# Kernel optimization log

Hardware: AMD Instinct MI355X
Metric: run time of the kernel (lower is better)

Reference implementation:

```python
import jax, jax.numpy as jnp
import numpy as np

ATOMF_LEN = 82
EDGE_DIM = 6
HIDDEN = 10
GNN_DEPTH = 2
N_NODES = 200000
N_EDGES = 6400000


def _lrelu(x):
    return jax.nn.leaky_relu(x, negative_slope=0.1)


def setup_inputs() -> dict:
    key = jax.random.key(0)
    ks = jax.random.split(key, 7)
    vertex = jax.random.normal(ks[0], (N_NODES, ATOMF_LEN), dtype=jnp.float32)
    edge_feat = jax.random.normal(ks[1], (N_EDGES, EDGE_DIM), dtype=jnp.float32)
    src = jax.random.randint(ks[2], (N_EDGES,), 0, N_NODES, dtype=jnp.int32)
    dst = jax.random.randint(ks[3], (N_EDGES,), 0, N_NODES, dtype=jnp.int32)
    # kaiming-uniform-ish init scale (fan_in based)
    weight_init = jax.random.uniform(ks[4], (ATOMF_LEN, HIDDEN), dtype=jnp.float32,
                                     minval=-1.0, maxval=1.0) * (np.sqrt(6.0 / ATOMF_LEN))
    gather_weight = jax.random.uniform(ks[5], (HIDDEN + EDGE_DIM, HIDDEN), dtype=jnp.float32,
                                       minval=-1.0, maxval=1.0) * (np.sqrt(6.0 / (HIDDEN + EDGE_DIM)))
    update_weight = jax.random.uniform(ks[6], (2 * HIDDEN, HIDDEN), dtype=jnp.float32,
                                       minval=-1.0, maxval=1.0) * (np.sqrt(6.0 / (2 * HIDDEN)))
    return {"vertex": vertex, "edge_feat": edge_feat, "src": src, "dst": dst,
            "weight_init": weight_init, "gather_weight": gather_weight,
            "update_weight": update_weight}


def reference(vertex, edge_feat, src, dst, weight_init, gather_weight, update_weight):
    # embedding_: leaky_relu(mm(x, W), 0.1)
    h = _lrelu(vertex @ weight_init)  # [N, HIDDEN]
    n_nodes = vertex.shape[0]
    for _ in range(GNN_DEPTH):
        # gather: per-edge message from source node hidden + edge features
        msg = _lrelu(jnp.concatenate([h[src], edge_feat], axis=1) @ gather_weight)  # [E, HIDDEN]
        # scatter-sum aggregation onto destination nodes
        agg = jax.ops.segment_sum(msg, dst, num_segments=n_nodes)  # [N, HIDDEN]
        # update: combine current hidden with aggregated messages
        h = _lrelu(jnp.concatenate([h, agg], axis=1) @ update_weight)  # [N, HIDDEN]
    return h
```

## Files before the change

kernel.cpp:

```cpp
#include <hip/hip_runtime.h>

#define ATOMF 82
#define EDGE_DIM 6
#define HIDDEN 10
#define ZPAD 16

#define BSHIFT 8
#define MAXBUCK 1024
#define NB1 1024
#define MAXE3 16384

__device__ __forceinline__ float lrelu(float x) { return x > 0.f ? x : 0.1f * x; }

__device__ __forceinline__ unsigned int f2bf(float f) {
    unsigned int u = __float_as_uint(f);
    return (u + 0x7fffu + ((u >> 16) & 1u)) >> 16;
}
__device__ __forceinline__ float bf2f(unsigned int b) {
    return __uint_as_float(b << 16);
}

__global__ void embed_kernel(const float* __restrict__ vertex,
                             const float* __restrict__ W,
                             const float* __restrict__ GW,
                             float* __restrict__ h, unsigned short* __restrict__ z,
                             int n_nodes) {
    __shared__ float w[ATOMF * HIDDEN];
    __shared__ float gwh[HIDDEN * HIDDEN];
    for (int i = threadIdx.x; i < ATOMF * HIDDEN; i += blockDim.x) w[i] = W[i];
    for (int i = threadIdx.x; i < HIDDEN * HIDDEN; i += blockDim.x) gwh[i] = GW[i];
    __syncthreads();
    int node = blockIdx.x * blockDim.x + threadIdx.x;
    if (node >= n_nodes) return;
    const float2* v = (const float2*)(vertex + (long)node * ATOMF);
    float acc[HIDDEN];
#pragma unroll
    for (int j = 0; j < HIDDEN; j++) acc[j] = 0.f;
#pragma unroll 2
    for (int k2 = 0; k2 < ATOMF / 2; k2++) {
        float2 t = v[k2];
#pragma unroll
        for (int j = 0; j < HIDDEN; j++) acc[j] += t.x * w[(2 * k2) * HIDDEN + j];
#pragma unroll
        for (int j = 0; j < HIDDEN; j++) acc[j] += t.y * w[(2 * k2 + 1) * HIDDEN + j];
    }
    float ho[HIDDEN];
    float* out = h + (long)node * HIDDEN;
#pragma unroll
    for (int j = 0; j < HIDDEN; j++) { ho[j] = lrelu(acc[j]); out[j] = ho[j]; }
    float zv[HIDDEN];
#pragma unroll
    for (int j = 0; j < HIDDEN; j++) zv[j] = 0.f;
#pragma unroll
    for (int k = 0; k < HIDDEN; k++) {
        float x = ho[k];
#pragma unroll
        for (int j = 0; j < HIDDEN; j++) zv[j] += x * gwh[k * HIDDEN + j];
    }
    unsigned int* zq = (unsigned int*)(z + (size_t)node * ZPAD);
    int4 pk;
    pk.x = (int)(f2bf(zv[0]) | (f2bf(zv[1]) << 16));
    pk.y = (int)(f2bf(zv[2]) | (f2bf(zv[3]) << 16));
    pk.z = (int)(f2bf(zv[4]) | (f2bf(zv[5]) << 16));
    pk.w = (int)(f2bf(zv[6]) | (f2bf(zv[7]) << 16));
    *(int4*)zq = pk;
    zq[4] = f2bf(zv[8]) | (f2bf(zv[9]) << 16);
}

__global__ __launch_bounds__(256) void hist_kernel(const int* __restrict__ dst,
                                                   int* __restrict__ hist,
                                                   long n_edges, int nbuck) {
    __shared__ int hl[MAXBUCK];
    for (int t = threadIdx.x; t < nbuck; t += 256) hl[t] = 0;
    __syncthreads();
    long per = (n_edges + gridDim.x - 1) / gridDim.x;
    long s = (long)blockIdx.x * per;
    long e = s + per; if (e > n_edges) e = n_edges;
    for (long i = s + threadIdx.x; i < e; i += 256)
        atomicAdd(&hl[dst[i] >> BSHIFT], 1);
    __syncthreads();
    for (int t = threadIdx.x; t < nbuck; t += 256)
        hist[(size_t)t * gridDim.x + blockIdx.x] = hl[t];
}

__global__ __launch_bounds__(1024) void scan_block_sums(const int* __restrict__ in,
                                                        int* __restrict__ partials, int n) {
    __shared__ int ws[16];
    int i = blockIdx.x * 1024 + threadIdx.x;
    int v = (i < n) ? in[i] : 0;
    int lane = threadIdx.x & 63, wid = threadIdx.x >> 6;
    int s = v;
#pragma unroll
    for (int off = 32; off > 0; off >>= 1) s += __shfl_down(s, off, 64);
    if (lane == 0) ws[wid] = s;
    __syncthreads();
    if (threadIdx.x == 0) {
        int t = 0;
#pragma unroll
        for (int k = 0; k < 16; k++) t += ws[k];
        partials[blockIdx.x] = t;
    }
}
__global__ __launch_bounds__(1024) void scan_partials(int* __restrict__ partials, int nb) {
    __shared__ int wsum[16];
    int lane = threadIdx.x & 63, wid = threadIdx.x >> 6;
    int v = (threadIdx.x < nb) ? partials[threadIdx.x] : 0;
    int incl = v;
#pragma unroll
    for (int off = 1; off < 64; off <<= 1) {
        int t = __shfl_up(incl, off, 64);
        if (lane >= off) incl += t;
    }
    if (lane == 63) wsum[wid] = incl;
    __syncthreads();
    if (wid == 0 && lane < 16) {
        int wv = wsum[lane];
        int wincl = wv;
#pragma unroll
        for (int off = 1; off < 16; off <<= 1) {
            int t = __shfl_up(wincl, off, 64);
            if (lane >= off) wincl += t;
        }
        wsum[lane] = wincl - wv;
    }
    __syncthreads();
    if (threadIdx.x < nb) partials[threadIdx.x] = wsum[wid] + (incl - v);
}
__global__ __launch_bounds__(1024) void scan_final(const int* __restrict__ in,
                                                   const int* __restrict__ partials,
                                                   int* __restrict__ out, int n) {
    __shared__ int wsum[16];
    int i = blockIdx.x * 1024 + threadIdx.x;
    int v = (i < n) ? in[i] : 0;
    int lane = threadIdx.x & 63, wid = threadIdx.x >> 6;
    int incl = v;
#pragma unroll
    for (int off = 1; off < 64; off <<= 1) {
        int t = __shfl_up(incl, off, 64);
        if (lane >= off) incl += t;
    }
    if (lane == 63) wsum[wid] = incl;
    __syncthreads();
    if (wid == 0 && lane < 16) {
        int wv = wsum[lane];
        int wincl = wv;
#pragma unroll
        for (int off = 1; off < 16; off <<= 1) {
            int t = __shfl_up(wincl, off, 64);
            if (lane >= off) wincl += t;
        }
        wsum[lane] = wincl - wv;
    }
    __syncthreads();
    if (i <= n) out[i] = partials[blockIdx.x] + wsum[wid] + (incl - v);
}

__global__ __launch_bounds__(256) void part_scatter_kernel(
    const int* __restrict__ src, const int* __restrict__ dst,
    const float* __restrict__ ef, const int* __restrict__ base,
    int4* __restrict__ rec_a, int* __restrict__ dst2,
    long n_edges, int nbuck) {
    __shared__ int cur[MAXBUCK];
    for (int t = threadIdx.x; t < nbuck; t += 256)
        cur[t] = base[(size_t)t * gridDim.x + blockIdx.x];
    __syncthreads();
    long per = (n_edges + gridDim.x - 1) / gridDim.x;
    long s = (long)blockIdx.x * per;
    long e = s + per; if (e > n_edges) e = n_edges;
    for (long i = s + threadIdx.x; i < e; i += 256) {
        int d = dst[i];
        int slot = atomicAdd(&cur[d >> BSHIFT], 1);
        const float2* er = (const float2*)(ef + i * (long)EDGE_DIM);
        float2 fa = er[0], fb = er[1], fc = er[2];
        int4 r;
        r.x = src[i];
        r.y = (int)(f2bf(fa.x) | (f2bf(fa.y) << 16));
        r.z = (int)(f2bf(fb.x) | (f2bf(fb.y) << 16));
        r.w = (int)(f2bf(fc.x) | (f2bf(fc.y) << 16));
        rec_a[slot] = r;
        dst2[slot] = d;
    }
}

__global__ __launch_bounds__(256) void bucket_csr_kernel(
    const int* __restrict__ base, const int* __restrict__ dst2,
    const int4* __restrict__ rec_a, int4* __restrict__ rec_b,
    int* __restrict__ offsets, int n_nodes) {
    __shared__ unsigned char lid[MAXE3];
    __shared__ int cnt[1 << BSHIFT];
    __shared__ int excl_s[1 << BSHIFT];
    __shared__ int cursor[1 << BSHIFT];
    int b = blockIdx.x;
    int S = base[(size_t)b * NB1];
    int E = base[(size_t)(b + 1) * NB1];
    int node0 = b << BSHIFT;
    int nn = n_nodes - node0; if (nn > (1 << BSHIFT)) nn = 1 << BSHIFT;
    cnt[threadIdx.x] = 0;
    __syncthreads();
    int ne = E - S;
    bool fit = (ne <= MAXE3);
    for (int i = threadIdx.x; i < ne; i += 256) {
        int l = dst2[S + i] - node0;
        if (fit) lid[i] = (unsigned char)l;
        atomicAdd(&cnt[l], 1);
    }
    __syncthreads();
    if (threadIdx.x == 0) {
        int run = 0;
#pragma unroll 4
        for (int l = 0; l < (1 << BSHIFT); l++) { excl_s[l] = run; run += cnt[l]; }
    }
    __syncthreads();
    if ((int)threadIdx.x < nn) offsets[node0 + threadIdx.x] = S + excl_s[threadIdx.x];
    cursor[threadIdx.x] = excl_s[threadIdx.x];
    if (b == (int)gridDim.x - 1 && threadIdx.x == 0) offsets[n_nodes] = E;
    __syncthreads();
    for (int i = threadIdx.x; i < ne; i += 256) {
        int l = fit ? (int)lid[i] : (dst2[S + i] - node0);
        int r = atomicAdd(&cursor[l], 1);
        rec_b[S + r] = rec_a[S + i];
    }
}

__global__ void count_pos_kernel(const int* __restrict__ dst, int* __restrict__ counts,
                                 unsigned short* __restrict__ pos, long n_edges) {
    long e0 = ((long)blockIdx.x * blockDim.x + threadIdx.x) * 4;
    if (e0 + 3 < n_edges) {
        int4 d = *(const int4*)(dst + e0);
        ushort4 p;
        p.x = (unsigned short)atomicAdd(&counts[d.x], 1);
        p.y = (unsigned short)atomicAdd(&counts[d.y], 1);
        p.z = (unsigned short)atomicAdd(&counts[d.z], 1);
        p.w = (unsigned short)atomicAdd(&counts[d.w], 1);
        *(ushort4*)(pos + e0) = p;
    } else {
        for (long e = e0; e < n_edges; e++)
            pos[e] = (unsigned short)atomicAdd(&counts[dst[e]], 1);
    }
}
__global__ void scatter_rec_kernel(const int* __restrict__ src, const int* __restrict__ dst,
                                   const float* __restrict__ ef,
                                   const unsigned short* __restrict__ pos,
                                   const int* __restrict__ offsets,
                                   int4* __restrict__ rec, long n_edges) {
    long e = (long)blockIdx.x * blockDim.x + threadIdx.x;
    if (e >= n_edges) return;
    int d = dst[e];
    int q = offsets[d] + (int)pos[e];
    const float2* er = (const float2*)(ef + e * (long)EDGE_DIM);
    float2 fa = er[0], fb = er[1], fc = er[2];
    int4 r;
    r.x = src[e];
    r.y = (int)(f2bf(fa.x) | (f2bf(fa.y) << 16));
    r.z = (int)(f2bf(fb.x) | (f2bf(fb.y) << 16));
    r.w = (int)(f2bf(fc.x) | (f2bf(fc.y) << 16));
    rec[q] = r;
}

__global__ __launch_bounds__(256) void gather_update_kernel(
    const float* __restrict__ h_in, const unsigned short* __restrict__ z_in,
    const int4* __restrict__ rec, const int* __restrict__ offsets,
    const float* __restrict__ GW, const float* __restrict__ UW,
    float* __restrict__ h_out, unsigned short* __restrict__ z_out,
    int n_nodes, int write_z) {
    __shared__ float gwh[HIDDEN * HIDDEN];
    __shared__ float gwe[EDGE_DIM * HIDDEN];
    __shared__ float uw[2 * HIDDEN * HIDDEN];
    for (int i = threadIdx.x; i < HIDDEN * HIDDEN; i += 256) gwh[i] = GW[i];
    for (int i = threadIdx.x; i < EDGE_DIM * HIDDEN; i += 256) gwe[i] = GW[HIDDEN * HIDDEN + i];
    for (int i = threadIdx.x; i < 2 * HIDDEN * HIDDEN; i += 256) uw[i] = UW[i];
    __syncthreads();
    int group = threadIdx.x >> 4;
    int sub = threadIdx.x & 15;
    int node = blockIdx.x * 16 + group;
    if (node >= n_nodes) return;
    int off0 = offsets[node], off1 = offsets[node + 1];
    float acc[HIDDEN];
#pragma unroll
    for (int j = 0; j < HIDDEN; j++) acc[j] = 0.f;
    int p = off0 + sub;
    int4 r;
    if (p < off1) r = rec[p];
    while (p < off1) {
        int pn = p + 16;
        int4 rn = r;
        if (pn < off1) rn = rec[pn];
        const int* zq = (const int*)(z_in + (size_t)r.x * ZPAD);
        int4 za = *(const int4*)zq;
        int zb = zq[4];
        float ef[EDGE_DIM];
        unsigned int u0 = (unsigned int)r.y, u1 = (unsigned int)r.z, u2 = (unsigned int)r.w;
        ef[0] = bf2f(u0 & 0xffffu); ef[1] = bf2f(u0 >> 16);
        ef[2] = bf2f(u1 & 0xffffu); ef[3] = bf2f(u1 >> 16);
        ef[4] = bf2f(u2 & 0xffffu); ef[5] = bf2f(u2 >> 16);
        float m[HIDDEN];
#pragma unroll
        for (int j = 0; j < HIDDEN; j++) m[j] = 0.f;
#pragma unroll
        for (int k = 0; k < EDGE_DIM; k++) {
            float x = ef[k];
#pragma unroll
            for (int j = 0; j < HIDDEN; j++) m[j] += x * gwe[k * HIDDEN + j];
        }
        unsigned int z0 = (unsigned int)za.x, z1 = (unsigned int)za.y;
        unsigned int z2 = (unsigned int)za.z, z3 = (unsigned int)za.w, z4 = (unsigned int)zb;
        acc[0] += lrelu(m[0] + bf2f(z0 & 0xffffu));
        acc[1] += lrelu(m[1] + bf2f(z0 >> 16));
        acc[2] += lrelu(m[2] + bf2f(z1 & 0xffffu));
        acc[3] += lrelu(m[3] + bf2f(z1 >> 16));
        acc[4] += lrelu(m[4] + bf2f(z2 & 0xffffu));
        acc[5] += lrelu(m[5] + bf2f(z2 >> 16));
        acc[6] += lrelu(m[6] + bf2f(z3 & 0xffffu));
        acc[7] += lrelu(m[7] + bf2f(z3 >> 16));
        acc[8] += lrelu(m[8] + bf2f(z4 & 0xffffu));
        acc[9] += lrelu(m[9] + bf2f(z4 >> 16));
        r = rn; p = pn;
    }
#pragma unroll
    for (int j = 0; j < HIDDEN; j++) {
#pragma unroll
        for (int d = 8; d > 0; d >>= 1) acc[j] += __shfl_down(acc[j], d, 16);
    }
    if (sub == 0) {
        float in[2 * HIDDEN];
        const float2* hp = (const float2*)(h_in + (long)node * HIDDEN);
#pragma unroll
        for (int k = 0; k < 5; k++) { float2 t = hp[k]; in[2 * k] = t.x; in[2 * k + 1] = t.y; }
#pragma unroll
        for (int j = 0; j < HIDDEN; j++) in[HIDDEN + j] = acc[j];
        float o[HIDDEN];
#pragma unroll
        for (int j = 0; j < HIDDEN; j++) o[j] = 0.f;
#pragma unroll
        for (int k = 0; k < 2 * HIDDEN; k++) {
            float x = in[k];
#pragma unroll
            for (int j = 0; j < HIDDEN; j++) o[j] += x * uw[k * HIDDEN + j];
        }
        float ho[HIDDEN];
        float* outp = h_out + (long)node * HIDDEN;
#pragma unroll
        for (int j = 0; j < HIDDEN; j++) { ho[j] = lrelu(o[j]); outp[j] = ho[j]; }
        if (write_z) {
            float zv[HIDDEN];
#pragma unroll
            for (int j = 0; j < HIDDEN; j++) zv[j] = 0.f;
#pragma unroll
            for (int k = 0; k < HIDDEN; k++) {
                float x = ho[k];
#pragma unroll
                for (int j = 0; j < HIDDEN; j++) zv[j] += x * gwh[k * HIDDEN + j];
            }
            unsigned int* zq = (unsigned int*)(z_out + (size_t)node * ZPAD);
            int4 pk;
            pk.x = (int)(f2bf(zv[0]) | (f2bf(zv[1]) << 16));
            pk.y = (int)(f2bf(zv[2]) | (f2bf(zv[3]) << 16));
            pk.z = (int)(f2bf(zv[4]) | (f2bf(zv[5]) << 16));
            pk.w = (int)(f2bf(zv[6]) | (f2bf(zv[7]) << 16));
            *(int4*)zq = pk;
            zq[4] = f2bf(zv[8]) | (f2bf(zv[9]) << 16);
        }
    }
}

extern "C" void kernel_launch(void* const* d_in, const int* in_sizes, int n_in,
                              void* d_out, int out_size, void* d_ws, size_t ws_size,
                              hipStream_t stream) {
    const float* vertex    = (const float*)d_in[0];
    const float* edge_feat = (const float*)d_in[1];
    const int*   src       = (const int*)d_in[2];
    const int*   dst       = (const int*)d_in[3];
    const float* w_init    = (const float*)d_in[4];
    const float* gw        = (const float*)d_in[5];
    const float* uw        = (const float*)d_in[6];

    const int  n_nodes = in_sizes[0] / ATOMF;
    const long n_edges = (long)in_sizes[2];
    float* out = (float*)d_out;

    const int TB = 256;
    const int node_blocks = (n_nodes + TB - 1) / TB;
    const int gu_blocks   = (n_nodes + 15) / 16;

    const int nbuck = (n_nodes + (1 << BSHIFT) - 1) >> BSHIFT;
    const long m = (long)nbuck * NB1;
    const int scanb_m = (int)((m + 1 + 1023) / 1024);

    size_t tbl_bytes = (size_t)n_nodes * (2 * HIDDEN * sizeof(float) + 2 * ZPAD * sizeof(unsigned short));
    size_t rec_bytes = (size_t)n_edges * sizeof(int4);

    auto al = [](size_t x) { return (x + 255) & ~(size_t)255; };
    size_t need_new = al(m * 4) + al((m + 1) * 4) + al(2048 * 4) +
                      al((size_t)(n_nodes + 1) * 4) + al(rec_bytes) +
                      al(rec_bytes > tbl_bytes ? rec_bytes : tbl_bytes) +
                      al((size_t)n_edges * 4);

    char* ws = (char*)d_ws;
    size_t o = 0;
    auto alloc = [&](size_t bytes) { char* p = ws + o; o = (o + bytes + 255) & ~(size_t)255; return p; };

    if (nbuck <= MAXBUCK && scanb_m <= 1024 && ws_size >= need_new) {
        int*  hist     = (int*)alloc(m * 4);
        int*  base     = (int*)alloc((m + 1) * 4);
        int*  partials = (int*)alloc(2048 * 4);
        int*  offsets  = (int*)alloc((size_t)(n_nodes + 1) * 4);
        int4* rec_b    = (int4*)alloc(rec_bytes);
        char* ovl      = alloc(rec_bytes > tbl_bytes ? rec_bytes : tbl_bytes);
        int4* rec_a    = (int4*)ovl;
        int*  dst2     = (int*)alloc((size_t)n_edges * 4);
        float*          h0 = (float*)ovl;
        float*          h1 = h0 + (size_t)n_nodes * HIDDEN;
        unsigned short* z0 = (unsigned short*)(h1 + (size_t)n_nodes * HIDDEN);
        unsigned short* z1 = z0 + (size_t)n_nodes * ZPAD;

        hipMemsetAsync(hist, 0, m * 4, stream);
        hist_kernel<<<NB1, 256, 0, stream>>>(dst, hist, n_edges, nbuck);
        scan_block_sums<<<scanb_m, 1024, 0, stream>>>(hist, partials, (int)m);
        scan_partials<<<1, 1024, 0, stream>>>(partials, scanb_m);
        scan_final<<<scanb_m, 1024, 0, stream>>>(hist, partials, base, (int)m);
        part_scatter_kernel<<<NB1, 256, 0, stream>>>(src, dst, edge_feat, base,
                                                     rec_a, dst2, n_edges, nbuck);
        bucket_csr_kernel<<<nbuck, 256, 0, stream>>>(base, dst2, rec_a, rec_b,
                                                     offsets, n_nodes);

        embed_kernel<<<node_blocks, TB, 0, stream>>>(vertex, w_init, gw, h0, z0, n_nodes);
        gather_update_kernel<<<gu_blocks, TB, 0, stream>>>(h0, z0, rec_b, offsets, gw, uw,
                                                           h1, z1, n_nodes, 1);
        gather_update_kernel<<<gu_blocks, TB, 0, stream>>>(h1, z1, rec_b, offsets, gw, uw,
                                                           out, z0, n_nodes, 0);
    } else {
        int*  counts   = (int*)alloc((size_t)(n_nodes + 1) * 4);
        int*  offsets  = (int*)alloc((size_t)(n_nodes + 1) * 4);
        int*  partials = (int*)alloc(2048 * 4);
        int4* rec      = (int4*)alloc(rec_bytes);
        size_t pos_bytes = (size_t)n_edges * sizeof(unsigned short);
        char* overlay = alloc(pos_bytes > tbl_bytes ? pos_bytes : tbl_bytes);
        unsigned short* pos = (unsigned short*)overlay;
        float*          h0  = (float*)overlay;
        float*          h1  = h0 + (size_t)n_nodes * HIDDEN;
        unsigned short* z0  = (unsigned short*)(h1 + (size_t)n_nodes * HIDDEN);
        unsigned short* z1  = z0 + (size_t)n_nodes * ZPAD;

        const int edge_blocks = (int)((n_edges + TB - 1) / TB);
        const int cp_blocks   = (int)((n_edges / 4 + TB - 1) / TB);
        const int scan_blocks = (n_nodes + 1 + 1023) / 1024;

        hipMemsetAsync(counts, 0, (size_t)(n_nodes + 1) * 4, stream);
        count_pos_kernel<<<cp_blocks, TB, 0, stream>>>(dst, counts, pos, n_edges);
        scan_block_sums<<<scan_blocks, 1024, 0, stream>>>(counts, partials, n_nodes);
        scan_partials<<<1, 1024, 0, stream>>>(partials, scan_blocks);
        scan_final<<<scan_blocks, 1024, 0, stream>>>(counts, partials, offsets, n_nodes);
        scatter_rec_kernel<<<edge_blocks, TB, 0, stream>>>(src, dst, edge_feat, pos, offsets,
                                                           rec, n_edges);
        embed_kernel<<<node_blocks, TB, 0, stream>>>(vertex, w_init, gw, h0, z0, n_nodes);
        gather_update_kernel<<<gu_blocks, TB, 0, stream>>>(h0, z0, rec, offsets, gw, uw,
                                                           h1, z1, n_nodes, 1);
        gather_update_kernel<<<gu_blocks, TB, 0, stream>>>(h1, z1, rec, offsets, gw, uw,
                                                           out, z0, n_nodes, 0);
    }
    (void)ws_size;
}
```

Before: 878.9 us.

## Drop per-node CSR pass; aggregate bucket-sorted edges with shared-memory atomics

Removes the second-level bucket_csr sort and the dst2 array by packing each edge's local destination index into the top 8 bits of the src field. A new gather_bucket_kernel processes one 256-node bucket per block, accumulates messages into shared memory with float atomics, then applies the update in-block. This cuts a full pass over the 6.4M edge records and the memset, at the cost of LDS atomic contention and up to 782 blocks with variable edge counts. The partition kernels also move to 256 blocks of 512 threads.

New measurement: 1.339 ms. +52.3%, slower.

```diff
diff --git a/kernel.cpp b/kernel.cpp
--- a/kernel.cpp
+++ b/kernel.cpp
@@ -6,9 +6,9 @@
 #define ZPAD 16
 
 #define BSHIFT 8
+#define BUCKN (1 << BSHIFT)
 #define MAXBUCK 1024
-#define NB1 1024
-#define MAXE3 16384
+#define NB2 256
 
 __device__ __forceinline__ float lrelu(float x) { return x > 0.f ? x : 0.1f * x; }
 
@@ -67,19 +67,19 @@
     zq[4] = f2bf(zv[8]) | (f2bf(zv[9]) << 16);
 }
 
-__global__ __launch_bounds__(256) void hist_kernel(const int* __restrict__ dst,
+__global__ __launch_bounds__(512) void hist_kernel(const int* __restrict__ dst,
                                                    int* __restrict__ hist,
                                                    long n_edges, int nbuck) {
     __shared__ int hl[MAXBUCK];
-    for (int t = threadIdx.x; t < nbuck; t += 256) hl[t] = 0;
+    for (int t = threadIdx.x; t < nbuck; t += 512) hl[t] = 0;
     __syncthreads();
     long per = (n_edges + gridDim.x - 1) / gridDim.x;
     long s = (long)blockIdx.x * per;
     long e = s + per; if (e > n_edges) e = n_edges;
-    for (long i = s + threadIdx.x; i < e; i += 256)
+    for (long i = s + threadIdx.x; i < e; i += 512)
         atomicAdd(&hl[dst[i] >> BSHIFT], 1);
     __syncthreads();
-    for (int t = threadIdx.x; t < nbuck; t += 256)
+    for (int t = threadIdx.x; t < nbuck; t += 512)
         hist[(size_t)t * gridDim.x + blockIdx.x] = hl[t];
 }
 
@@ -155,70 +155,134 @@
     if (i <= n) out[i] = partials[blockIdx.x] + wsum[wid] + (incl - v);
 }
 
-__global__ __launch_bounds__(256) void part_scatter_kernel(
+__global__ __launch_bounds__(512) void part_scatter_kernel(
     const int* __restrict__ src, const int* __restrict__ dst,
     const float* __restrict__ ef, const int* __restrict__ base,
-    int4* __restrict__ rec_a, int* __restrict__ dst2,
-    long n_edges, int nbuck) {
+    int4* __restrict__ rec, long n_edges, int nbuck) {
     __shared__ int cur[MAXBUCK];
-    for (int t = threadIdx.x; t < nbuck; t += 256)
+    for (int t = threadIdx.x; t < nbuck; t += 512)
         cur[t] = base[(size_t)t * gridDim.x + blockIdx.x];
     __syncthreads();
     long per = (n_edges + gridDim.x - 1) / gridDim.x;
     long s = (long)blockIdx.x * per;
     long e = s + per; if (e > n_edges) e = n_edges;
-    for (long i = s + threadIdx.x; i < e; i += 256) {
+    for (long i = s + threadIdx.x; i < e; i += 512) {
         int d = dst[i];
         int slot = atomicAdd(&cur[d >> BSHIFT], 1);
         const float2* er = (const float2*)(ef + i * (long)EDGE_DIM);
         float2 fa = er[0], fb = er[1], fc = er[2];
         int4 r;
-        r.x = src[i];
+        r.x = src[i] | ((d & (BUCKN - 1)) << 24);
         r.y = (int)(f2bf(fa.x) | (f2bf(fa.y) << 16));
         r.z = (int)(f2bf(fb.x) | (f2bf(fb.y) << 16));
         r.w = (int)(f2bf(fc.x) | (f2bf(fc.y) << 16));
-        rec_a[slot] = r;
-        dst2[slot] = d;
-    }
-}
-
-__global__ __launch_bounds__(256) void bucket_csr_kernel(
-    const int* __restrict__ base, const int* __restrict__ dst2,
-    const int4* __restrict__ rec_a, int4* __restrict__ rec_b,
-    int* __restrict__ offsets, int n_nodes) {
-    __shared__ unsigned char lid[MAXE3];
-    __shared__ int cnt[1 << BSHIFT];
-    __shared__ int excl_s[1 << BSHIFT];
-    __shared__ int cursor[1 << BSHIFT];
+        rec[slot] = r;
+    }
+}
+
+__global__ __launch_bounds__(512) void gather_bucket_kernel(
+    const float* __restrict__ h_in, const unsigned short* __restrict__ z_in,
+    const int4* __restrict__ rec, const int* __restrict__ base,
+    const float* __restrict__ GW, const float* __restrict__ UW,
+    float* __restrict__ h_out, unsigned short* __restrict__ z_out,
+    int n_nodes, int write_z) {
+    __shared__ float gwh[HIDDEN * HIDDEN];
+    __shared__ float gwe[EDGE_DIM * HIDDEN];
+    __shared__ float uw[2 * HIDDEN * HIDDEN];
+    __shared__ float acc[BUCKN * HIDDEN];
+    __shared__ float hl[BUCKN * HIDDEN];
+    for (int i = threadIdx.x; i < HIDDEN * HIDDEN; i += 512) gwh[i] = GW[i];
+    for (int i = threadIdx.x; i < EDGE_DIM * HIDDEN; i += 512) gwe[i] = GW[HIDDEN * HIDDEN + i];
+    for (int i = threadIdx.x; i < 2 * HIDDEN * HIDDEN; i += 512) uw[i] = UW[i];
+    for (int i = threadIdx.x; i < BUCKN * HIDDEN; i += 512) acc[i] = 0.f;
     int b = blockIdx.x;
-    int S = base[(size_t)b * NB1];
-    int E = base[(size_t)(b + 1) * NB1];
     int node0 = b << BSHIFT;
-    int nn = n_nodes - node0; if (nn > (1 << BSHIFT)) nn = 1 << BSHIFT;
-    cnt[threadIdx.x] = 0;
-    __syncthreads();
-    int ne = E - S;
-    bool fit = (ne <= MAXE3);
-    for (int i = threadIdx.x; i < ne; i += 256) {
-        int l = dst2[S + i] - node0;
-        if (fit) lid[i] = (unsigned char)l;
-        atomicAdd(&cnt[l], 1);
-    }
-    __syncthreads();
-    if (threadIdx.x == 0) {
-        int run = 0;
-#pragma unroll 4
-        for (int l = 0; l < (1 << BSHIFT); l++) { excl_s[l] = run; run += cnt[l]; }
-    }
-    __syncthreads();
-    if ((int)threadIdx.x < nn) offsets[node0 + threadIdx.x] = S + excl_s[threadIdx.x];
-    cursor[threadIdx.x] = excl_s[threadIdx.x];
-    if (b == (int)gridDim.x - 1 && threadIdx.x == 0) offsets[n_nodes] = E;
-    __syncthreads();
-    for (int i = threadIdx.x; i < ne; i += 256) {
-        int l = fit ? (int)lid[i] : (dst2[S + i] - node0);
-        int r = atomicAdd(&cursor[l], 1);
-        rec_b[S + r] = rec_a[S + i];
+    int nelem = (n_nodes - node0) * HIDDEN;
+    if (nelem > BUCKN * HIDDEN) nelem = BUCKN * HIDDEN;
+    for (int i = threadIdx.x; i < nelem; i += 512) hl[i] = h_in[(size_t)node0 * HIDDEN + i];
+    __syncthreads();
+    int S = base[(size_t)b * NB2];
+    int E = base[(size_t)(b + 1) * NB2];
+    for (int i = S + (int)threadIdx.x; i < E; i += 512) {
+        int4 r = rec[i];
+        unsigned int rx = (unsigned int)r.x;
+        int sn = (int)(rx & 0x00ffffffu);
+        int l = (int)(rx >> 24);
+        const int* zq = (const int*)(z_in + (size_t)sn * ZPAD);
+        int4 za = *(const int4*)zq;
+        int zb = zq[4];
+        float efv[EDGE_DIM];
+        unsigned int u0 = (unsigned int)r.y, u1 = (unsigned int)r.z, u2 = (unsigned int)r.w;
+        efv[0] = bf2f(u0 & 0xffffu); efv[1] = bf2f(u0 >> 16);
+        efv[2] = bf2f(u1 & 0xffffu); efv[3] = bf2f(u1 >> 16);
+        efv[4] = bf2f(u2 & 0xffffu); efv[5] = bf2f(u2 >> 16);
+        float m[HIDDEN];
+#pragma unroll
+        for (int j = 0; j < HIDDEN; j++) m[j] = 0.f;
+#pragma unroll
+        for (int k = 0; k < EDGE_DIM; k++) {
+            float x = efv[k];
+#pragma unroll
+            for (int j = 0; j < HIDDEN; j++) m[j] += x * gwe[k * HIDDEN + j];
+        }
+        unsigned int z0 = (unsigned int)za.x, z1 = (unsigned int)za.y;
+        unsigned int z2 = (unsigned int)za.z, z3 = (unsigned int)za.w, z4 = (unsigned int)zb;
+        float mg[HIDDEN];
+        mg[0] = lrelu(m[0] + bf2f(z0 & 0xffffu));
+        mg[1] = lrelu(m[1] + bf2f(z0 >> 16));
+        mg[2] = lrelu(m[2] + bf2f(z1 & 0xffffu));
+        mg[3] = lrelu(m[3] + bf2f(z1 >> 16));
+        mg[4] = lrelu(m[4] + bf2f(z2 & 0xffffu));
+        mg[5] = lrelu(m[5] + bf2f(z2 >> 16));
+        mg[6] = lrelu(m[6] + bf2f(z3 & 0xffffu));
+        mg[7] = lrelu(m[7] + bf2f(z3 >> 16));
+        mg[8] = lrelu(m[8] + bf2f(z4 & 0xffffu));
+        mg[9] = lrelu(m[9] + bf2f(z4 >> 16));
+        float* ap = acc + l * HIDDEN;
+#pragma unroll
+        for (int j = 0; j < HIDDEN; j++) atomicAdd(&ap[j], mg[j]);
+    }
+    __syncthreads();
+    int t = threadIdx.x;
+    int node = node0 + t;
+    if (t < BUCKN && node < n_nodes) {
+        float in[2 * HIDDEN];
+#pragma unroll
+        for (int k = 0; k < HIDDEN; k++) in[k] = hl[t * HIDDEN + k];
+#pragma unroll
+        for (int j = 0; j < HIDDEN; j++) in[HIDDEN + j] = acc[t * HIDDEN + j];
+        float o[HIDDEN];
+#pragma unroll
+        for (int j = 0; j < HIDDEN; j++) o[j] = 0.f;
+#pragma unroll
+        for (int k = 0; k < 2 * HIDDEN; k++) {
+            float x = in[k];
+#pragma unroll
+            for (int j = 0; j < HIDDEN; j++) o[j] += x * uw[k * HIDDEN + j];
+        }
+        float ho[HIDDEN];
+        float* outp = h_out + (size_t)node * HIDDEN;
+#pragma unroll
+        for (int j = 0; j < HIDDEN; j++) { ho[j] = lrelu(o[j]); outp[j] = ho[j]; }
+        if (write_z) {
+            float zv[HIDDEN];
+#pragma unroll
+            for (int j = 0; j < HIDDEN; j++) zv[j] = 0.f;
+#pragma unroll
+            for (int k = 0; k < HIDDEN; k++) {
+                float x = ho[k];
+#pragma unroll
+                for (int j = 0; j < HIDDEN; j++) zv[j] += x * gwh[k * HIDDEN + j];
+            }
+            unsigned int* zq = (unsigned int*)(z_out + (size_t)node * ZPAD);
+            int4 pk;
+            pk.x = (int)(f2bf(zv[0]) | (f2bf(zv[1]) << 16));
+            pk.y = (int)(f2bf(zv[2]) | (f2bf(zv[3]) << 16));
+            pk.z = (int)(f2bf(zv[4]) | (f2bf(zv[5]) << 16));
+            pk.w = (int)(f2bf(zv[6]) | (f2bf(zv[7]) << 16));
+            *(int4*)zq = pk;
+            zq[4] = f2bf(zv[8]) | (f2bf(zv[9]) << 16);
+        }
     }
 }
 
@@ -380,54 +444,44 @@
 
     const int TB = 256;
     const int node_blocks = (n_nodes + TB - 1) / TB;
-    const int gu_blocks   = (n_nodes + 15) / 16;
-
-    const int nbuck = (n_nodes + (1 << BSHIFT) - 1) >> BSHIFT;
-    const long m = (long)nbuck * NB1;
+
+    const int nbuck = (n_nodes + BUCKN - 1) >> BSHIFT;
+    const long m = (long)nbuck * NB2;
     const int scanb_m = (int)((m + 1 + 1023) / 1024);
 
     size_t tbl_bytes = (size_t)n_nodes * (2 * HIDDEN * sizeof(float) + 2 * ZPAD * sizeof(unsigned short));
     size_t rec_bytes = (size_t)n_edges * sizeof(int4);
 
     auto al = [](size_t x) { return (x + 255) & ~(size_t)255; };
-    size_t need_new = al(m * 4) + al((m + 1) * 4) + al(2048 * 4) +
-                      al((size_t)(n_nodes + 1) * 4) + al(rec_bytes) +
-                      al(rec_bytes > tbl_bytes ? rec_bytes : tbl_bytes) +
-                      al((size_t)n_edges * 4);
+    size_t need_new = al(m * 4) + al((m + 1) * 4) + al(2048 * 4) + al(rec_bytes) + al(tbl_bytes);
 
     char* ws = (char*)d_ws;
     size_t o = 0;
     auto alloc = [&](size_t bytes) { char* p = ws + o; o = (o + bytes + 255) & ~(size_t)255; return p; };
 
-    if (nbuck <= MAXBUCK && scanb_m <= 1024 && ws_size >= need_new) {
+    if (nbuck <= MAXBUCK && scanb_m <= 1024 && n_nodes <= (1 << 24) && ws_size >= need_new) {
         int*  hist     = (int*)alloc(m * 4);
         int*  base     = (int*)alloc((m + 1) * 4);
         int*  partials = (int*)alloc(2048 * 4);
-        int*  offsets  = (int*)alloc((size_t)(n_nodes + 1) * 4);
-        int4* rec_b    = (int4*)alloc(rec_bytes);
-        char* ovl      = alloc(rec_bytes > tbl_bytes ? rec_bytes : tbl_bytes);
-        int4* rec_a    = (int4*)ovl;
-        int*  dst2     = (int*)alloc((size_t)n_edges * 4);
-        float*          h0 = (float*)ovl;
+        int4* rec      = (int4*)alloc(rec_bytes);
+        char* tbl      = alloc(tbl_bytes);
+        float*          h0 = (float*)tbl;
         float*          h1 = h0 + (size_t)n_nodes * HIDDEN;
         unsigned short* z0 = (unsigned short*)(h1 + (size_t)n_nodes * HIDDEN);
         unsigned short* z1 = z0 + (size_t)n_nodes * ZPAD;
 
-        hipMemsetAsync(hist, 0, m * 4, stream);
-        hist_kernel<<<NB1, 256, 0, stream>>>(dst, hist, n_edges, nbuck);
+        hist_kernel<<<NB2, 512, 0, stream>>>(dst, hist, n_edges, nbuck);
         scan_block_sums<<<scanb_m, 1024, 0, stream>>>(hist, partials, (int)m);
         scan_partials<<<1, 1024, 0, stream>>>(partials, scanb_m);
         scan_final<<<scanb_m, 1024, 0, stream>>>(hist, partials, base, (int)m);
-        part_scatter_kernel<<<NB1, 256, 0, stream>>>(src, dst, edge_feat, base,
-                                                     rec_a, dst2, n_edges, nbuck);
-        bucket_csr_kernel<<<nbuck, 256, 0, stream>>>(base, dst2, rec_a, rec_b,
-                                                     offsets, n_nodes);
+        part_scatter_kernel<<<NB2, 512, 0, stream>>>(src, dst, edge_feat, base, rec,
+                                                     n_edges, nbuck);
 
         embed_kernel<<<node_blocks, TB, 0, stream>>>(vertex, w_init, gw, h0, z0, n_nodes);
-        gather_update_kernel<<<gu_blocks, TB, 0, stream>>>(h0, z0, rec_b, offsets, gw, uw,
-                                                           h1, z1, n_nodes, 1);
-        gather_update_kernel<<<gu_blocks, TB, 0, stream>>>(h1, z1, rec_b, offsets, gw, uw,
-                                                           out, z0, n_nodes, 0);
+        gather_bucket_kernel<<<nbuck, 512, 0, stream>>>(h0, z0, rec, base, gw, uw,
+                                                        h1, z1, n_nodes, 1);
+        gather_bucket_kernel<<<nbuck, 512, 0, stream>>>(h1, z1, rec, base, gw, uw,
+                                                        out, z0, n_nodes, 0);
     } else {
         int*  counts   = (int*)alloc((size_t)(n_nodes + 1) * 4);
         int*  offsets  = (int*)alloc((size_t)(n_nodes + 1) * 4);
@@ -444,6 +498,7 @@
         const int edge_blocks = (int)((n_edges + TB - 1) / TB);
         const int cp_blocks   = (int)((n_edges / 4 + TB - 1) / TB);
         const int scan_blocks = (n_nodes + 1 + 1023) / 1024;
+        const int gu_blocks   = (n_nodes + 15) / 16;
 
         hipMemsetAsync(counts, 0, (size_t)(n_nodes + 1) * 4, stream);
         count_pos_kernel<<<cp_blocks, TB, 0, stream>>>(dst, counts, pos, n_edges);
```

## Pack local dst into src high bits, drop dst2 array, shrink partition grid

Applied to the files above, without the earlier changes.

The partition scatter now stores the node index within its bucket in the top 8 bits of the record's src field, so the separate dst2 array is no longer written or read. The bucket CSR pass reads that byte back from the record, and the gather kernel masks it off. This saves one 4-byte-per-edge write and read stream. The partition histogram also moves from 1024 blocks of 256 threads to 256 blocks of 512 threads, which shrinks the histogram and scan table by 4x and drops the memset, but leaves fewer blocks on the edge passes and requires fewer than 2^24 nodes.

Measured after the change: 760.7 us. 1.16x faster.

```diff
diff --git a/kernel.cpp b/kernel.cpp
--- a/kernel.cpp
+++ b/kernel.cpp
@@ -6,8 +6,9 @@
 #define ZPAD 16
 
 #define BSHIFT 8
+#define BUCKN (1 << BSHIFT)
 #define MAXBUCK 1024
-#define NB1 1024
+#define NB2 256
 #define MAXE3 16384
 
 __device__ __forceinline__ float lrelu(float x) { return x > 0.f ? x : 0.1f * x; }
@@ -67,19 +68,19 @@
     zq[4] = f2bf(zv[8]) | (f2bf(zv[9]) << 16);
 }
 
-__global__ __launch_bounds__(256) void hist_kernel(const int* __restrict__ dst,
+__global__ __launch_bounds__(512) void hist_kernel(const int* __restrict__ dst,
                                                    int* __restrict__ hist,
                                                    long n_edges, int nbuck) {
     __shared__ int hl[MAXBUCK];
-    for (int t = threadIdx.x; t < nbuck; t += 256) hl[t] = 0;
+    for (int t = threadIdx.x; t < nbuck; t += 512) hl[t] = 0;
     __syncthreads();
     long per = (n_edges + gridDim.x - 1) / gridDim.x;
     long s = (long)blockIdx.x * per;
     long e = s + per; if (e > n_edges) e = n_edges;
-    for (long i = s + threadIdx.x; i < e; i += 256)
+    for (long i = s + threadIdx.x; i < e; i += 512)
         atomicAdd(&hl[dst[i] >> BSHIFT], 1);
     __syncthreads();
-    for (int t = threadIdx.x; t < nbuck; t += 256)
+    for (int t = threadIdx.x; t < nbuck; t += 512)
         hist[(size_t)t * gridDim.x + blockIdx.x] = hl[t];
 }
 
@@ -155,52 +156,49 @@
     if (i <= n) out[i] = partials[blockIdx.x] + wsum[wid] + (incl - v);
 }
 
-__global__ __launch_bounds__(256) void part_scatter_kernel(
+__global__ __launch_bounds__(512) void part_scatter_kernel(
     const int* __restrict__ src, const int* __restrict__ dst,
     const float* __restrict__ ef, const int* __restrict__ base,
-    int4* __restrict__ rec_a, int* __restrict__ dst2,
-    long n_edges, int nbuck) {
+    int4* __restrict__ rec, long n_edges, int nbuck) {
     __shared__ int cur[MAXBUCK];
-    for (int t = threadIdx.x; t < nbuck; t += 256)
+    for (int t = threadIdx.x; t < nbuck; t += 512)
         cur[t] = base[(size_t)t * gridDim.x + blockIdx.x];
     __syncthreads();
     long per = (n_edges + gridDim.x - 1) / gridDim.x;
     long s = (long)blockIdx.x * per;
     long e = s + per; if (e > n_edges) e = n_edges;
-    for (long i = s + threadIdx.x; i < e; i += 256) {
+    for (long i = s + threadIdx.x; i < e; i += 512) {
         int d = dst[i];
         int slot = atomicAdd(&cur[d >> BSHIFT], 1);
         const float2* er = (const float2*)(ef + i * (long)EDGE_DIM);
         float2 fa = er[0], fb = er[1], fc = er[2];
         int4 r;
-        r.x = src[i];
+        r.x = src[i] | ((d & (BUCKN - 1)) << 24);
         r.y = (int)(f2bf(fa.x) | (f2bf(fa.y) << 16));
         r.z = (int)(f2bf(fb.x) | (f2bf(fb.y) << 16));
         r.w = (int)(f2bf(fc.x) | (f2bf(fc.y) << 16));
-        rec_a[slot] = r;
-        dst2[slot] = d;
+        rec[slot] = r;
     }
 }
 
 __global__ __launch_bounds__(256) void bucket_csr_kernel(
-    const int* __restrict__ base, const int* __restrict__ dst2,
-    const int4* __restrict__ rec_a, int4* __restrict__ rec_b,
+    const int* __restrict__ base, const int4* __restrict__ rec_a, int4* __restrict__ rec_b,
     int* __restrict__ offsets, int n_nodes) {
     __shared__ unsigned char lid[MAXE3];
-    __shared__ int cnt[1 << BSHIFT];
-    __shared__ int excl_s[1 << BSHIFT];
-    __shared__ int cursor[1 << BSHIFT];
+    __shared__ int cnt[BUCKN];
+    __shared__ int excl_s[BUCKN];
+    __shared__ int cursor[BUCKN];
     int b = blockIdx.x;
-    int S = base[(size_t)b * NB1];
-    int E = base[(size_t)(b + 1) * NB1];
+    int S = base[(size_t)b * NB2];
+    int E = base[(size_t)(b + 1) * NB2];
     int node0 = b << BSHIFT;
-    int nn = n_nodes - node0; if (nn > (1 << BSHIFT)) nn = 1 << BSHIFT;
+    int nn = n_nodes - node0; if (nn > BUCKN) nn = BUCKN;
     cnt[threadIdx.x] = 0;
     __syncthreads();
     int ne = E - S;
     bool fit = (ne <= MAXE3);
     for (int i = threadIdx.x; i < ne; i += 256) {
-        int l = dst2[S + i] - node0;
+        int l = (int)((unsigned int)rec_a[S + i].x >> 24);
         if (fit) lid[i] = (unsigned char)l;
         atomicAdd(&cnt[l], 1);
     }
@@ -208,7 +206,7 @@
     if (threadIdx.x == 0) {
         int run = 0;
 #pragma unroll 4
-        for (int l = 0; l < (1 << BSHIFT); l++) { excl_s[l] = run; run += cnt[l]; }
+        for (int l = 0; l < BUCKN; l++) { excl_s[l] = run; run += cnt[l]; }
     }
     __syncthreads();
     if ((int)threadIdx.x < nn) offsets[node0 + threadIdx.x] = S + excl_s[threadIdx.x];
@@ -216,9 +214,10 @@
     if (b == (int)gridDim.x - 1 && threadIdx.x == 0) offsets[n_nodes] = E;
     __syncthreads();
     for (int i = threadIdx.x; i < ne; i += 256) {
-        int l = fit ? (int)lid[i] : (dst2[S + i] - node0);
-        int r = atomicAdd(&cursor[l], 1);
-        rec_b[S + r] = rec_a[S + i];
+        int4 r = rec_a[S + i];
+        int l = fit ? (int)lid[i] : (int)((unsigned int)r.x >> 24);
+        int q = atomicAdd(&cursor[l], 1);
+        rec_b[S + q] = r;
     }
 }
 
@@ -262,7 +261,7 @@
     const int4* __restrict__ rec, const int* __restrict__ offsets,
     const float* __restrict__ GW, const float* __restrict__ UW,
     float* __restrict__ h_out, unsigned short* __restrict__ z_out,
-    int n_nodes, int write_z) {
+    int n_nodes, int write_z, unsigned int src_mask) {
     __shared__ float gwh[HIDDEN * HIDDEN];
     __shared__ float gwe[EDGE_DIM * HIDDEN];
     __shared__ float uw[2 * HIDDEN * HIDDEN];
@@ -285,7 +284,8 @@
         int pn = p + 16;
         int4 rn = r;
         if (pn < off1) rn = rec[pn];
-        const int* zq = (const int*)(z_in + (size_t)r.x * ZPAD);
+        int sn = (int)((unsigned int)r.x & src_mask);
+        const int* zq = (const int*)(z_in + (size_t)sn * ZPAD);
         int4 za = *(const int4*)zq;
         int zb = zq[4];
         float ef[EDGE_DIM];
@@ -382,8 +382,8 @@
     const int node_blocks = (n_nodes + TB - 1) / TB;
     const int gu_blocks   = (n_nodes + 15) / 16;
 
-    const int nbuck = (n_nodes + (1 << BSHIFT) - 1) >> BSHIFT;
-    const long m = (long)nbuck * NB1;
+    const int nbuck = (n_nodes + BUCKN - 1) >> BSHIFT;
+    const long m = (long)nbuck * NB2;
     const int scanb_m = (int)((m + 1 + 1023) / 1024);
 
     size_t tbl_bytes = (size_t)n_nodes * (2 * HIDDEN * sizeof(float) + 2 * ZPAD * sizeof(unsigned short));
@@ -392,14 +392,13 @@
     auto al = [](size_t x) { return (x + 255) & ~(size_t)255; };
     size_t need_new = al(m * 4) + al((m + 1) * 4) + al(2048 * 4) +
                       al((size_t)(n_nodes + 1) * 4) + al(rec_bytes) +
-                      al(rec_bytes > tbl_bytes ? rec_bytes : tbl_bytes) +
-                      al((size_t)n_edges * 4);
+                      al(rec_bytes > tbl_bytes ? rec_bytes : tbl_bytes);
 
     char* ws = (char*)d_ws;
     size_t o = 0;
     auto alloc = [&](size_t bytes) { char* p = ws + o; o = (o + bytes + 255) & ~(size_t)255; return p; };
 
-    if (nbuck <= MAXBUCK && scanb_m <= 1024 && ws_size >= need_new) {
+    if (nbuck <= MAXBUCK && scanb_m <= 1024 && n_nodes <= (1 << 24) && ws_size >= need_new) {
         int*  hist     = (int*)alloc(m * 4);
         int*  base     = (int*)alloc((m + 1) * 4);
         int*  partials = (int*)alloc(2048 * 4);
@@ -407,27 +406,24 @@
         int4* rec_b    = (int4*)alloc(rec_bytes);
         char* ovl      = alloc(rec_bytes > tbl_bytes ? rec_bytes : tbl_bytes);
         int4* rec_a    = (int4*)ovl;
-        int*  dst2     = (int*)alloc((size_t)n_edges * 4);
         float*          h0 = (float*)ovl;
         float*          h1 = h0 + (size_t)n_nodes * HIDDEN;
         unsigned short* z0 = (unsigned short*)(h1 + (size_t)n_nodes * HIDDEN);
         unsigned short* z1 = z0 + (size_t)n_nodes * ZPAD;
 
-        hipMemsetAsync(hist, 0, m * 4, stream);
-        hist_kernel<<<NB1, 256, 0, stream>>>(dst, hist, n_edges, nbuck);
+        hist_kernel<<<NB2, 512, 0, stream>>>(dst, hist, n_edges, nbuck);
         scan_block_sums<<<scanb_m, 1024, 0, stream>>>(hist, partials, (int)m);
         scan_partials<<<1, 1024, 0, stream>>>(partials, scanb_m);
         scan_final<<<scanb_m, 1024, 0, stream>>>(hist, partials, base, (int)m);
-        part_scatter_kernel<<<NB1, 256, 0, stream>>>(src, dst, edge_feat, base,
-                                                     rec_a, dst2, n_edges, nbuck);
-        bucket_csr_kernel<<<nbuck, 256, 0, stream>>>(base, dst2, rec_a, rec_b,
-                                                     offsets, n_nodes);
+        part_scatter_kernel<<<NB2, 512, 0, stream>>>(src, dst, edge_feat, base, rec_a,
+                                                     n_edges, nbuck);
+        bucket_csr_kernel<<<nbuck, 256, 0, stream>>>(base, rec_a, rec_b, offsets, n_nodes);
 
         embed_kernel<<<node_blocks, TB, 0, stream>>>(vertex, w_init, gw, h0, z0, n_nodes);
         gather_update_kernel<<<gu_blocks, TB, 0, stream>>>(h0, z0, rec_b, offsets, gw, uw,
-                                                           h1, z1, n_nodes, 1);
+                                                           h1, z1, n_nodes, 1, 0x00ffffffu);
         gather_update_kernel<<<gu_blocks, TB, 0, stream>>>(h1, z1, rec_b, offsets, gw, uw,
-                                                           out, z0, n_nodes, 0);
+                                                           out, z0, n_nodes, 0, 0x00ffffffu);
     } else {
         int*  counts   = (int*)alloc((size_t)(n_nodes + 1) * 4);
         int*  offsets  = (int*)alloc((size_t)(n_nodes + 1) * 4);
@@ -454,9 +450,9 @@
                                                            rec, n_edges);
         embed_kernel<<<node_blocks, TB, 0, stream>>>(vertex, w_init, gw, h0, z0, n_nodes);
         gather_update_kernel<<<gu_blocks, TB, 0, stream>>>(h0, z0, rec, offsets, gw, uw,
-                                                           h1, z1, n_nodes, 1);
+                                                           h1, z1, n_nodes, 1, 0xffffffffu);
         gather_update_kernel<<<gu_blocks, TB, 0, stream>>>(h1, z1, rec, offsets, gw, uw,
-                                                           out, z0, n_nodes, 0);
+                                                           out, z0, n_nodes, 0, 0xffffffffu);
     }
     (void)ws_size;
 }
```
